# Kernel optimization log

Measured on AMD Instinct MI355X. Metric: run time of the kernel, lower is better.

## Reference

```python
import jax, jax.numpy as jnp
import numpy as np

D_MODEL = 1024
NUM_HEADS = 16
HEAD_DIM = D_MODEL // NUM_HEADS
BATCH, SEQ = 2, 2048


def setup_inputs() -> dict:
    key = jax.random.key(0)
    ks = jax.random.split(key, 5)
    scale = 1.0 / np.sqrt(D_MODEL)  # ~xavier magnitude
    x = jax.random.normal(ks[0], (BATCH, SEQ, D_MODEL), dtype=jnp.float32)
    Wq = jax.random.normal(ks[1], (D_MODEL, D_MODEL), dtype=jnp.float32) * scale
    Wk = jax.random.normal(ks[2], (D_MODEL, D_MODEL), dtype=jnp.float32) * scale
    Wv = jax.random.normal(ks[3], (D_MODEL, D_MODEL), dtype=jnp.float32) * scale
    Wo = jax.random.normal(ks[4], (D_MODEL, D_MODEL), dtype=jnp.float32) * scale
    z = jnp.zeros((D_MODEL,), dtype=jnp.float32)
    return {"x": x, "Wq": Wq, "bq": z, "Wk": Wk, "bk": z, "Wv": Wv, "bv": z, "Wo": Wo, "bo": z}


def reference(x, Wq, bq, Wk, bk, Wv, bv, Wo, bo):
    B, S, _ = x.shape
    H, Dh = NUM_HEADS, HEAD_DIM
    # torch Linear convention: y = x @ W^T + b
    q = (x @ Wq.T + bq).reshape(B, S, H, Dh)
    k = (x @ Wk.T + bk).reshape(B, S, H, Dh)
    v = (x @ Wv.T + bv).reshape(B, S, H, Dh)
    # scores: [B, H, S, S]
    scores = jnp.einsum('bqhd,bkhd->bhqk', q, k) / np.sqrt(Dh).astype(np.float32)
    attn = jax.nn.softmax(scores, axis=-1)
    out = jnp.einsum('bhqk,bkhd->bqhd', attn, v).reshape(B, S, H * Dh)
    return out @ Wo.T + bo
```

## Files before the change

kernel.cpp:

```cpp
#include <hip/hip_runtime.h>
#include <hip/hip_bf16.h>

typedef __bf16 bf16;
typedef __bf16 bf16x8 __attribute__((ext_vector_type(8)));
typedef __bf16 bf16x4 __attribute__((ext_vector_type(4)));
typedef float f32x4 __attribute__((ext_vector_type(4)));

constexpr int DM = 1024, NH = 16, DH = 64, NB = 2, SQ = 2048;
constexpr int MTOT = NB * SQ;
constexpr float QSCALE = 0.125f * 1.44269504088896f;

__device__ __forceinline__ void gld_lds16(const bf16* g, bf16* l) {
  __builtin_amdgcn_global_load_lds(
      (const __attribute__((address_space(1))) void*)g,
      (__attribute__((address_space(3))) void*)l, 16, 0, 0);
}

__global__ __launch_bounds__(256) void cvt5(
    const float* __restrict__ s0, const float* __restrict__ s1,
    const float* __restrict__ s2, const float* __restrict__ s3,
    const float* __restrict__ s4,
    bf16* __restrict__ d0, bf16* __restrict__ d1, bf16* __restrict__ d2,
    bf16* __restrict__ d3, bf16* __restrict__ d4) {
  const int idx = (blockIdx.x * 256 + threadIdx.x) * 4;
  const float* src; bf16* dst; int off;
  if (idx < 4 * DM * DM) {
    off = idx & (DM * DM - 1);
    switch (idx >> 20) {
      case 0: src = s0; dst = d0; break;
      case 1: src = s1; dst = d1; break;
      case 2: src = s2; dst = d2; break;
      default: src = s3; dst = d3; break;
    }
  } else {
    src = s4; dst = d4; off = idx - 4 * DM * DM;
  }
  const float4 v = *(const float4*)(src + off);
  *(bf16x4*)(dst + off) = (bf16x4){(bf16)v.x, (bf16)v.y, (bf16)v.z, (bf16)v.w};
}

template <int BM, typename OutT>
__device__ __forceinline__ void gemm_tile(
    const bf16* __restrict__ A, const bf16* __restrict__ Bm,
    const float* __restrict__ bias, OutT* __restrict__ C,
    int rowA0, int rowB0, int N, int K, bool bias_row, float cscale,
    bf16* sA, bf16* sB) {
  constexpr int NT = (BM == 128) ? 4 : 2;
  const int tid = threadIdx.x;
  const int wave = tid >> 6, lane = tid & 63;
  const int quad = lane >> 4, l16 = lane & 15;
  const int row0w = (BM == 128) ? (wave >> 1) * 64 : 0;
  const int col0w = (BM == 128) ? (wave & 1) * 64 : wave * 32;

  f32x4 acc[4][NT];
#pragma unroll
  for (int i = 0; i < 4; i++)
#pragma unroll
    for (int j = 0; j < NT; j++) acc[i][j] = (f32x4){0.f, 0.f, 0.f, 0.f};

  const int srow = lane >> 3;
  const int scol = ((lane & 7) ^ srow) * 8;

  for (int kt = 0; kt < K; kt += 64) {
#pragma unroll
    for (int i = 0; i < BM / 32; i++) {
      const int r = i * 32 + wave * 8;
      gld_lds16(A + (size_t)(rowA0 + r + srow) * K + kt + scol, &sA[r * 64]);
    }
#pragma unroll
    for (int i = 0; i < 4; i++) {
      const int r = i * 32 + wave * 8;
      gld_lds16(Bm + (size_t)(rowB0 + r + srow) * K + kt + scol, &sB[r * 64]);
    }
    __syncthreads();
#pragma unroll
    for (int kk = 0; kk < 64; kk += 32) {
      bf16x8 aF[4], bF[NT];
      const int slot = (((kk >> 3) + quad) ^ (l16 & 7)) << 3;
#pragma unroll
      for (int mt = 0; mt < 4; mt++)
        aF[mt] = *(const bf16x8*)&sA[(row0w + mt * 16 + l16) * 64 + slot];
#pragma unroll
      for (int nt = 0; nt < NT; nt++)
        bF[nt] = *(const bf16x8*)&sB[(col0w + nt * 16 + l16) * 64 + slot];
#pragma unroll
      for (int mt = 0; mt < 4; mt++)
#pragma unroll
        for (int nt = 0; nt < NT; nt++)
          acc[mt][nt] = __builtin_amdgcn_mfma_f32_16x16x32_bf16(aF[mt], bF[nt], acc[mt][nt], 0, 0, 0);
    }
    __syncthreads();
  }

#pragma unroll
  for (int mt = 0; mt < 4; mt++) {
#pragma unroll
    for (int nt = 0; nt < NT; nt++) {
#pragma unroll
      for (int r = 0; r < 4; r++) {
        const int row = rowA0 + row0w + mt * 16 + quad * 4 + r;
        const int col = rowB0 + col0w + nt * 16 + l16;
        const float bb = bias_row ? bias[row] : bias[col];
        C[(size_t)row * N + col] = (OutT)((acc[mt][nt][r] + bb) * cscale);
      }
    }
  }
}

__global__ __launch_bounds__(256, 4) void qkv_gemm(
    const bf16* __restrict__ xb, const bf16* __restrict__ Wqb,
    const bf16* __restrict__ Wkb, const bf16* __restrict__ Wvb,
    const float* __restrict__ bq, const float* __restrict__ bk,
    const float* __restrict__ bv,
    bf16* __restrict__ Qw, bf16* __restrict__ Kw, bf16* __restrict__ VTw) {
  __shared__ alignas(16) bf16 sA[128 * 64];
  __shared__ alignas(16) bf16 sB[128 * 64];
  if (blockIdx.z == 0) {
    gemm_tile<128, bf16>(xb, Wqb, bq, Qw, blockIdx.x * 128, blockIdx.y * 128, DM, DM, false, QSCALE, sA, sB);
  } else if (blockIdx.z == 1) {
    gemm_tile<128, bf16>(xb, Wkb, bk, Kw, blockIdx.x * 128, blockIdx.y * 128, DM, DM, false, 1.0f, sA, sB);
  } else {
    const int id = blockIdx.y * 32 + blockIdx.x;
    gemm_tile<128, bf16>(Wvb, xb, bv, VTw, (id >> 5) * 128, (id & 31) * 128, MTOT, DM, true, 1.0f, sA, sB);
  }
}

__global__ __launch_bounds__(256, 4) void out_gemm(
    const bf16* __restrict__ A, const bf16* __restrict__ Bm,
    const float* __restrict__ bias, float* __restrict__ C) {
  __shared__ alignas(16) bf16 sA[64 * 64];
  __shared__ alignas(16) bf16 sB[128 * 64];
  gemm_tile<64, float>(A, Bm, bias, C, blockIdx.x * 64, blockIdx.y * 128, DM, DM, false, 1.0f, sA, sB);
}

__global__ __launch_bounds__(256, 4) void attn(
    const bf16* __restrict__ Q, const bf16* __restrict__ Kq,
    const bf16* __restrict__ VT, bf16* __restrict__ O) {
  __shared__ alignas(16) bf16 sK[2][64 * 64];
  __shared__ alignas(16) bf16 sV[2][64 * 64];
  __shared__ alignas(16) bf16 sP[4][16 * 64];
  const int tid = threadIdx.x, wave = tid >> 6, lane = tid & 63;
  const int quad = lane >> 4, l16 = lane & 15;
  const int hb = blockIdx.x, qt = blockIdx.y;
  const int h = hb & 15, b = hb >> 4;

  const bf16* Qg = Q + (size_t)(b * SQ + qt * 64) * DM + h * DH;
  const bf16* Kg = Kq + (size_t)(b * SQ) * DM + h * DH;
  const bf16* Vg = VT + (size_t)(h * DH) * MTOT + b * SQ;

  const int srow = lane >> 3, scol = ((lane & 7) ^ srow) * 8;

  auto stageKV = [&](int t, int buf) {
#pragma unroll
    for (int i = 0; i < 2; i++) {
      const int r = (wave * 2 + i) * 8;
      gld_lds16(Kg + (size_t)(t * 64 + r + srow) * DM + scol, &sK[buf][r * 64]);
    }
#pragma unroll
    for (int i = 0; i < 2; i++) {
      const int r = (wave * 2 + i) * 8;
      gld_lds16(Vg + (size_t)(r + srow) * MTOT + t * 64 + scol, &sV[buf][r * 64]);
    }
  };

  bf16x8 qF[2];
#pragma unroll
  for (int kkh = 0; kkh < 2; kkh++)
    qF[kkh] = *(const bf16x8*)(Qg + (size_t)(wave * 16 + l16) * DM + kkh * 32 + quad * 8);

  bf16x8 onesF;
#pragma unroll
  for (int i = 0; i < 8; i++) onesF[i] = (bf16)1.0f;

  f32x4 l_acc = (f32x4){0.f, 0.f, 0.f, 0.f};
  f32x4 o_acc[4];
#pragma unroll
  for (int n2 = 0; n2 < 4; n2++) o_acc[n2] = (f32x4){0.f, 0.f, 0.f, 0.f};

  stageKV(0, 0);
  for (int t = 0; t < 32; ++t) {
    __syncthreads();
    if (t + 1 < 32) stageKV(t + 1, (t + 1) & 1);
    const bf16* cK = sK[t & 1];
    const bf16* cV = sV[t & 1];

    f32x4 sacc[4];
#pragma unroll
    for (int nt = 0; nt < 4; nt++) sacc[nt] = (f32x4){0.f, 0.f, 0.f, 0.f};
#pragma unroll
    for (int kk = 0; kk < 64; kk += 32) {
      bf16x8 kF[4];
      const int slot = (((kk >> 3) + quad) ^ (l16 & 7)) << 3;
#pragma unroll
      for (int nt = 0; nt < 4; nt++)
        kF[nt] = *(const bf16x8*)&cK[(nt * 16 + l16) * 64 + slot];
      __builtin_amdgcn_s_setprio(1);
#pragma unroll
      for (int nt = 0; nt < 4; nt++)
        sacc[nt] = __builtin_amdgcn_mfma_f32_16x16x32_bf16(kF[nt], qF[kk >> 5],
                                                           sacc[nt], 0, 0, 0);
      __builtin_amdgcn_s_setprio(0);
    }

    const int prow = l16;
#pragma unroll
    for (int nt = 0; nt < 4; nt++) {
      const f32x4 s = sacc[nt];
      bf16x4 pk;
#pragma unroll
      for (int r = 0; r < 4; r++) pk[r] = (bf16)__builtin_amdgcn_exp2f(s[r]);
      const int c = 2 * nt + (quad >> 1);
      *(bf16x4*)&sP[wave][prow * 64 + ((c ^ (prow & 7)) << 3) + (quad & 1) * 4] = pk;
    }

#pragma unroll
    for (int kk = 0; kk < 64; kk += 32) {
      bf16x8 pF, vF[4];
      const int c = (kk >> 3) + quad;
      pF = *(const bf16x8*)&sP[wave][prow * 64 + ((c ^ (prow & 7)) << 3)];
      const int slot = (((kk >> 3) + quad) ^ (l16 & 7)) << 3;
#pragma unroll
      for (int n2 = 0; n2 < 4; n2++)
        vF[n2] = *(const bf16x8*)&cV[(n2 * 16 + l16) * 64 + slot];
      __builtin_amdgcn_s_setprio(1);
#pragma unroll
      for (int n2 = 0; n2 < 4; n2++)
        o_acc[n2] = __builtin_amdgcn_mfma_f32_16x16x32_bf16(pF, vF[n2], o_acc[n2], 0, 0, 0);
      l_acc = __builtin_amdgcn_mfma_f32_16x16x32_bf16(pF, onesF, l_acc, 0, 0, 0);
      __builtin_amdgcn_s_setprio(0);
    }
  }

#pragma unroll
  for (int r = 0; r < 4; r++) {
    const float inv = 1.0f / l_acc[r];
    const int row = qt * 64 + wave * 16 + quad * 4 + r;
#pragma unroll
    for (int n2 = 0; n2 < 4; n2++) {
      const int col = n2 * 16 + l16;
      O[(size_t)(b * SQ + row) * DM + h * DH + col] = (bf16)(o_acc[n2][r] * inv);
    }
  }
}

extern "C" void kernel_launch(void* const* d_in, const int* in_sizes, int n_in,
                              void* d_out, int out_size, void* d_ws, size_t ws_size,
                              hipStream_t stream) {
  const float* x  = (const float*)d_in[0];
  const float* Wq = (const float*)d_in[1];
  const float* bq = (const float*)d_in[2];
  const float* Wk = (const float*)d_in[3];
  const float* bk = (const float*)d_in[4];
  const float* Wv = (const float*)d_in[5];
  const float* bv = (const float*)d_in[6];
  const float* Wo = (const float*)d_in[7];
  const float* bo = (const float*)d_in[8];
  float* out = (float*)d_out;

  bf16* ws   = (bf16*)d_ws;
  bf16* xb   = ws;
  bf16* Wqb  = ws + (size_t)MTOT * DM;
  bf16* Wkb  = Wqb + (size_t)DM * DM;
  bf16* Wvb  = Wkb + (size_t)DM * DM;
  bf16* Wob  = Wvb + (size_t)DM * DM;
  bf16* Qw   = Wob + (size_t)DM * DM;
  bf16* Kw   = Qw + (size_t)MTOT * DM;
  bf16* VTw  = Kw + (size_t)MTOT * DM;
  bf16* Cw   = VTw + (size_t)MTOT * DM;

  const dim3 blk(256);
  cvt5<<<dim3((4 * DM * DM + MTOT * DM) / 1024, 1), blk, 0, stream>>>(
      Wq, Wk, Wv, Wo, x, Wqb, Wkb, Wvb, Wob, xb);
  qkv_gemm<<<dim3(32, 8, 3), blk, 0, stream>>>(xb, Wqb, Wkb, Wvb, bq, bk, bv, Qw, Kw, VTw);
  attn<<<dim3(NH * NB, SQ / 64), blk, 0, stream>>>(Qw, Kw, VTw, Cw);
  out_gemm<<<dim3(MTOT / 64, DM / 128), blk, 0, stream>>>(Cw, Wob, bo, out);
}
```

Baseline: 188.1 us.

## Rewrite attention with 32x32x16 MFMA, register P, and 128-row query tiles

The attention kernel moves from 16x16x32 to 32x32x16 MFMA tiles, with each wave owning 32 query rows and each block 128 rows, which halves the grid. The P matrix no longer goes through LDS: it is packed to bf16 in registers and rearranged across half-waves with permlane32 swaps. The row sum is now accumulated in scalar registers, replacing the extra ones-matrix MFMA. This removes LDS round-trips and redundant MFMA work and reuses each K/V tile across more queries, at the cost of higher register pressure (launch bounds drop to 2 blocks) and fewer blocks in flight.

```diff
diff --git a/kernel.cpp b/kernel.cpp
--- a/kernel.cpp
+++ b/kernel.cpp
@@ -5,6 +5,8 @@
 typedef __bf16 bf16x8 __attribute__((ext_vector_type(8)));
 typedef __bf16 bf16x4 __attribute__((ext_vector_type(4)));
 typedef float f32x4 __attribute__((ext_vector_type(4)));
+typedef float f32x16 __attribute__((ext_vector_type(16)));
+typedef unsigned int u32x4 __attribute__((ext_vector_type(4)));
 
 constexpr int DM = 1024, NH = 16, DH = 64, NB = 2, SQ = 2048;
 constexpr int MTOT = NB * SQ;
@@ -133,18 +135,17 @@
   gemm_tile<64, float>(A, Bm, bias, C, blockIdx.x * 64, blockIdx.y * 128, DM, DM, false, 1.0f, sA, sB);
 }
 
-__global__ __launch_bounds__(256, 4) void attn(
+__global__ __launch_bounds__(256, 2) void attn(
     const bf16* __restrict__ Q, const bf16* __restrict__ Kq,
     const bf16* __restrict__ VT, bf16* __restrict__ O) {
   __shared__ alignas(16) bf16 sK[2][64 * 64];
   __shared__ alignas(16) bf16 sV[2][64 * 64];
-  __shared__ alignas(16) bf16 sP[4][16 * 64];
   const int tid = threadIdx.x, wave = tid >> 6, lane = tid & 63;
-  const int quad = lane >> 4, l16 = lane & 15;
+  const int l32 = lane & 31, half = lane >> 5;
   const int hb = blockIdx.x, qt = blockIdx.y;
   const int h = hb & 15, b = hb >> 4;
 
-  const bf16* Qg = Q + (size_t)(b * SQ + qt * 64) * DM + h * DH;
+  const bf16* Qg = Q + (size_t)(b * SQ + qt * 128 + wave * 32) * DM + h * DH;
   const bf16* Kg = Kq + (size_t)(b * SQ) * DM + h * DH;
   const bf16* Vg = VT + (size_t)(h * DH) * MTOT + b * SQ;
 
@@ -155,27 +156,21 @@
     for (int i = 0; i < 2; i++) {
       const int r = (wave * 2 + i) * 8;
       gld_lds16(Kg + (size_t)(t * 64 + r + srow) * DM + scol, &sK[buf][r * 64]);
-    }
-#pragma unroll
-    for (int i = 0; i < 2; i++) {
-      const int r = (wave * 2 + i) * 8;
       gld_lds16(Vg + (size_t)(r + srow) * MTOT + t * 64 + scol, &sV[buf][r * 64]);
     }
   };
 
-  bf16x8 qF[2];
-#pragma unroll
-  for (int kkh = 0; kkh < 2; kkh++)
-    qF[kkh] = *(const bf16x8*)(Qg + (size_t)(wave * 16 + l16) * DM + kkh * 32 + quad * 8);
-
-  bf16x8 onesF;
-#pragma unroll
-  for (int i = 0; i < 8; i++) onesF[i] = (bf16)1.0f;
-
-  f32x4 l_acc = (f32x4){0.f, 0.f, 0.f, 0.f};
-  f32x4 o_acc[4];
-#pragma unroll
-  for (int n2 = 0; n2 < 4; n2++) o_acc[n2] = (f32x4){0.f, 0.f, 0.f, 0.f};
+  bf16x8 qF[4];
+#pragma unroll
+  for (int kk = 0; kk < 4; kk++)
+    qF[kk] = *(const bf16x8*)(Qg + (size_t)l32 * DM + kk * 16 + half * 8);
+
+  f32x16 o_acc[2];
+#pragma unroll
+  for (int nd = 0; nd < 2; nd++)
+#pragma unroll
+    for (int i = 0; i < 16; i++) o_acc[nd][i] = 0.f;
+  float lsum = 0.f;
 
   stageKV(0, 0);
   for (int t = 0; t < 32; ++t) {
@@ -183,62 +178,75 @@
     if (t + 1 < 32) stageKV(t + 1, (t + 1) & 1);
     const bf16* cK = sK[t & 1];
     const bf16* cV = sV[t & 1];
-
-    f32x4 sacc[4];
-#pragma unroll
-    for (int nt = 0; nt < 4; nt++) sacc[nt] = (f32x4){0.f, 0.f, 0.f, 0.f};
-#pragma unroll
-    for (int kk = 0; kk < 64; kk += 32) {
-      bf16x8 kF[4];
-      const int slot = (((kk >> 3) + quad) ^ (l16 & 7)) << 3;
-#pragma unroll
-      for (int nt = 0; nt < 4; nt++)
-        kF[nt] = *(const bf16x8*)&cK[(nt * 16 + l16) * 64 + slot];
-      __builtin_amdgcn_s_setprio(1);
-#pragma unroll
-      for (int nt = 0; nt < 4; nt++)
-        sacc[nt] = __builtin_amdgcn_mfma_f32_16x16x32_bf16(kF[nt], qF[kk >> 5],
-                                                           sacc[nt], 0, 0, 0);
-      __builtin_amdgcn_s_setprio(0);
-    }
-
-    const int prow = l16;
-#pragma unroll
-    for (int nt = 0; nt < 4; nt++) {
-      const f32x4 s = sacc[nt];
-      bf16x4 pk;
-#pragma unroll
-      for (int r = 0; r < 4; r++) pk[r] = (bf16)__builtin_amdgcn_exp2f(s[r]);
-      const int c = 2 * nt + (quad >> 1);
-      *(bf16x4*)&sP[wave][prow * 64 + ((c ^ (prow & 7)) << 3) + (quad & 1) * 4] = pk;
-    }
-
-#pragma unroll
-    for (int kk = 0; kk < 64; kk += 32) {
-      bf16x8 pF, vF[4];
-      const int c = (kk >> 3) + quad;
-      pF = *(const bf16x8*)&sP[wave][prow * 64 + ((c ^ (prow & 7)) << 3)];
-      const int slot = (((kk >> 3) + quad) ^ (l16 & 7)) << 3;
-#pragma unroll
-      for (int n2 = 0; n2 < 4; n2++)
-        vF[n2] = *(const bf16x8*)&cV[(n2 * 16 + l16) * 64 + slot];
-      __builtin_amdgcn_s_setprio(1);
-#pragma unroll
-      for (int n2 = 0; n2 < 4; n2++)
-        o_acc[n2] = __builtin_amdgcn_mfma_f32_16x16x32_bf16(pF, vF[n2], o_acc[n2], 0, 0, 0);
-      l_acc = __builtin_amdgcn_mfma_f32_16x16x32_bf16(pF, onesF, l_acc, 0, 0, 0);
-      __builtin_amdgcn_s_setprio(0);
-    }
-  }
-
-#pragma unroll
-  for (int r = 0; r < 4; r++) {
-    const float inv = 1.0f / l_acc[r];
-    const int row = qt * 64 + wave * 16 + quad * 4 + r;
-#pragma unroll
-    for (int n2 = 0; n2 < 4; n2++) {
-      const int col = n2 * 16 + l16;
-      O[(size_t)(b * SQ + row) * DM + h * DH + col] = (bf16)(o_acc[n2][r] * inv);
+    const int sw7 = l32 & 7;
+
+    f32x16 sacc[2];
+#pragma unroll
+    for (int nt = 0; nt < 2; nt++)
+#pragma unroll
+      for (int i = 0; i < 16; i++) sacc[nt][i] = 0.f;
+
+    bf16x8 kf[2][4];
+#pragma unroll
+    for (int nt = 0; nt < 2; nt++)
+#pragma unroll
+      for (int kk = 0; kk < 4; kk++)
+        kf[nt][kk] = *(const bf16x8*)&cK[(nt * 32 + l32) * 64 + (((kk * 2 + half) ^ sw7) << 3)];
+    __builtin_amdgcn_s_setprio(1);
+#pragma unroll
+    for (int nt = 0; nt < 2; nt++)
+#pragma unroll
+      for (int kk = 0; kk < 4; kk++)
+        sacc[nt] = __builtin_amdgcn_mfma_f32_32x32x16_bf16(kf[nt][kk], qF[kk], sacc[nt], 0, 0, 0);
+    __builtin_amdgcn_s_setprio(0);
+
+#pragma unroll
+    for (int nt = 0; nt < 2; nt++) {
+      float p[16];
+#pragma unroll
+      for (int i = 0; i < 16; i++) {
+        p[i] = __builtin_amdgcn_exp2f(sacc[nt][i]);
+        lsum += p[i];
+      }
+      unsigned int w[8];
+#pragma unroll
+      for (int i = 0; i < 8; i++)
+        asm("v_cvt_pk_bf16_f32 %0, %1, %2" : "=v"(w[i]) : "v"(p[2 * i]), "v"(p[2 * i + 1]));
+      asm("v_permlane32_swap_b32 %0, %1" : "+v"(w[0]), "+v"(w[2]));
+      asm("v_permlane32_swap_b32 %0, %1" : "+v"(w[1]), "+v"(w[3]));
+      asm("v_permlane32_swap_b32 %0, %1" : "+v"(w[4]), "+v"(w[6]));
+      asm("v_permlane32_swap_b32 %0, %1" : "+v"(w[5]), "+v"(w[7]));
+#pragma unroll
+      for (int s = 0; s < 2; s++) {
+        const u32x4 pw = (s == 0) ? (u32x4){w[0], w[1], w[2], w[3]}
+                                  : (u32x4){w[4], w[5], w[6], w[7]};
+        const bf16x8 pb = __builtin_bit_cast(bf16x8, pw);
+        const int ks = nt * 2 + s;
+        bf16x8 vf[2];
+#pragma unroll
+        for (int nd = 0; nd < 2; nd++)
+          vf[nd] = *(const bf16x8*)&cV[(nd * 32 + l32) * 64 + (((ks * 2 + half) ^ sw7) << 3)];
+        __builtin_amdgcn_s_setprio(1);
+#pragma unroll
+        for (int nd = 0; nd < 2; nd++)
+          o_acc[nd] = __builtin_amdgcn_mfma_f32_32x32x16_bf16(vf[nd], pb, o_acc[nd], 0, 0, 0);
+        __builtin_amdgcn_s_setprio(0);
+      }
+    }
+  }
+
+  const float lother = __shfl(lsum, lane ^ 32, 64);
+  const float inv = 1.0f / (lsum + lother);
+
+  bf16* Op = O + (size_t)(b * SQ + qt * 128 + wave * 32 + l32) * DM + h * DH;
+#pragma unroll
+  for (int nd = 0; nd < 2; nd++) {
+#pragma unroll
+    for (int g = 0; g < 4; g++) {
+      bf16x4 ov;
+#pragma unroll
+      for (int r = 0; r < 4; r++) ov[r] = (bf16)(o_acc[nd][g * 4 + r] * inv);
+      *(bf16x4*)(Op + nd * 32 + g * 8 + half * 4) = ov;
     }
   }
 }
@@ -272,6 +280,6 @@
   cvt5<<<dim3((4 * DM * DM + MTOT * DM) / 1024, 1), blk, 0, stream>>>(
       Wq, Wk, Wv, Wo, x, Wqb, Wkb, Wvb, Wob, xb);
   qkv_gemm<<<dim3(32, 8, 3), blk, 0, stream>>>(xb, Wqb, Wkb, Wvb, bq, bk, bv, Qw, Kw, VTw);
-  attn<<<dim3(NH * NB, SQ / 64), blk, 0, stream>>>(Qw, Kw, VTw, Cw);
+  attn<<<dim3(NH * NB, SQ / 128), blk, 0, stream>>>(Qw, Kw, VTw, Cw);
   out_gemm<<<dim3(MTOT / 64, DM / 128), blk, 0, stream>>>(Cw, Wob, bo, out);
 }
```

After: 180.5 us. -4.0%, faster.
